# Kernel tuning notes

Measured on AMD Instinct MI355X. Metric: run time of the kernel, lower is better.

Reference implementation:

```python
import jax, jax.numpy as jnp
import numpy as np

B, H, W = 4, 256, 256
TARGET_BETA0 = 5
TARGET_LIFETIME = 0.5
LOSS_SCALE = 100.0


def setup_inputs() -> dict:
    key = jax.random.key(0)
    k1, k2 = jax.random.split(key)
    prob_map = jax.random.uniform(k1, (B, 1, H, W), dtype=jnp.float32)
    roi_mask = (jax.random.uniform(k2, (B, 1, H, W)) < 0.9).astype(jnp.float32)
    return {"prob_map": prob_map, "roi_mask": roi_mask}


def _ph0_topk_loss(f):
    """0-dim persistent homology (V-filtration, 4-connectivity) of f:[H,W],
    then standard top-k MSE(target_lifetime) loss. Equivalent to
    cripser.compute_ph_torch(f, maxdim=0, filtration='V') + _standard_loss.
    Algorithm: Kruskal over grid edges with weight max(f[u],f[v]), elder rule.
    All combinatorics run on stop_gradient values; births/deaths are
    differentiable gathers from f at the paired pixel indices."""
    Hh, Ww = f.shape
    N = Hh * Ww
    fv = f.reshape(-1)
    fvc = jax.lax.stop_gradient(fv)

    idx2d = jnp.arange(N, dtype=jnp.int32).reshape(Hh, Ww)
    r_u = idx2d[:, :-1].reshape(-1)  # right edges
    r_v = r_u + 1
    d_u = idx2d[:-1, :].reshape(-1)  # down edges
    d_v = d_u + Ww
    eu = jnp.concatenate([r_u, d_u])
    ev = jnp.concatenate([r_v, d_v])
    ew = jnp.maximum(fvc[eu], fvc[ev])
    order = jnp.argsort(ew)  # process edges by increasing filtration value
    eu, ev = eu[order], ev[order]

    parent0 = jnp.arange(N, dtype=jnp.int32)

    def step(parent, uv):
        u, v = uv[0], uv[1]

        def find(x):
            return jax.lax.while_loop(lambda y: parent[y] != y, lambda y: parent[y], x)

        ru = find(u)
        rv = find(v)
        merge = ru != rv
        # Invariant: a root is the argmin pixel of its component, so
        # fvc[root] is the component's birth value. Elder rule: the root
        # with smaller birth value survives (ties -> smaller index).
        older_u = (fvc[ru] < fvc[rv]) | ((fvc[ru] == fvc[rv]) & (ru < rv))
        keep = jnp.where(older_u, ru, rv)
        die = jnp.where(older_u, rv, ru)
        b_idx = jnp.where(merge, die, -1)  # birth pixel of the dying comp
        d_pix = jnp.where(fvc[u] >= fvc[v], u, v)  # death = max endpoint
        d_idx = jnp.where(merge, d_pix, -1)
        parent = parent.at[die].set(jnp.where(merge, keep, die))
        parent = parent.at[u].set(jnp.where(merge, keep, ru))  # path compression
        parent = parent.at[v].set(jnp.where(merge, keep, rv))
        return parent, (b_idx, d_idx)

    _, (pb, pd_) = jax.lax.scan(step, parent0, jnp.stack([eu, ev], axis=1))

    valid = pb >= 0
    births = fv[jnp.maximum(pb, 0)]
    deaths = fv[jnp.maximum(pd_, 0)]
    life = jnp.where(valid, deaths - births, 0.0)  # lifetimes >= 0

    # sort descending; invalid slots to the end (keys are stop-gradient)
    key_ = jnp.where(valid, jax.lax.stop_gradient(life), -jnp.inf)
    top = jnp.argsort(-key_)[:TARGET_BETA0]
    topk = life[top]
    vk = valid[top]
    n_use = jnp.sum(vk)  # = min(num_finite, target_beta0)
    sq = jnp.where(vk, (topk - TARGET_LIFETIME) ** 2, 0.0)
    return jnp.sum(sq) / jnp.maximum(n_use, 1).astype(f.dtype)


def reference(prob_map, roi_mask):
    prob = prob_map[:, 0] * roi_mask[:, 0]  # roi masking; (1-roi)*0 is a no-op
    filtration = 1.0 - prob
    losses = jax.vmap(_ph0_topk_loss)(filtration)
    return jnp.mean(losses) * LOSS_SCALE
```

## Files before the change

### kernel.cpp

```cpp
#include <hip/hip_runtime.h>
#include <stdint.h>

#define NPIX 65536
#define NRE  65280
#define NE   130560
#define NIMG 4
#define LTPB 1024
#define ETPB 1024
#define NBLK_L (NIMG*32)
#define TPIX 2048
#define EPAD 4096
#define KMAX 4096
#define HSZ  1024
#define LHSZ 2048
typedef unsigned long long u64;

__device__ __forceinline__ int ufind(unsigned* lbl, int x){
  int r = x, c = (int)lbl[r];
  while (c != r){ r = c; c = (int)lbl[r]; }
  while ((int)lbl[x] != r){ int n = (int)lbl[x]; lbl[x] = (unsigned)r; x = n; }
  return r;
}
__device__ __forceinline__ int ufind16(unsigned short* uf, int x){
  int r = x, c = (int)uf[r];
  while (c != r){ r = c; c = (int)uf[r]; }
  while ((int)uf[x] != r){ int n = (int)uf[x]; uf[x] = (unsigned short)r; x = n; }
  return r;
}

__device__ __forceinline__ void merge5(float* a, const float* b){
  float out[5]; int ia = 0, ib = 0;
  #pragma unroll
  for (int k = 0; k < 5; ++k){
    float av = (ia < 5) ? a[ia] : -2.0f;
    float bv = (ib < 5) ? b[ib] : -2.0f;
    if (av >= bv){ out[k] = av; ++ia; } else { out[k] = bv; ++ib; }
  }
  #pragma unroll
  for (int k = 0; k < 5; ++k) a[k] = out[k];
}

__global__ __launch_bounds__(LTPB)
void ph0_local(const float* __restrict__ prob, const float* __restrict__ roi,
               float* __restrict__ Fg, float* __restrict__ LIFEg,
               unsigned* __restrict__ LBLg, u64* __restrict__ LAg,
               unsigned* __restrict__ C, unsigned* __restrict__ C2,
               unsigned* __restrict__ MAPg, unsigned* __restrict__ KGg)
{
  const int blk = blockIdx.x;
  const int img = blk >> 5;
  const int tile = blk & 31;
  const int tr = tile >> 2, tc = tile & 3;
  const int gr0 = tr*32, gc0 = tc*64;
  const int tid = threadIdx.x;
  const int lane = tid & 63;

  const float* pm = prob + img*NPIX;
  const float* rm = roi  + img*NPIX;
  float* F = Fg + img*NPIX;
  float* LIFE = LIFEg + img*NPIX;
  unsigned* LBL = LBLg + img*NPIX;
  unsigned* MAP = MAPg + img*NPIX;
  unsigned* KG  = KGg  + img*NPIX;
  u64* LA = LAg + (size_t)img*NE;

  __shared__ float          sf[TPIX];
  __shared__ unsigned       slbl[TPIX];
  __shared__ unsigned       sme[TPIX];
  __shared__ unsigned short el[2][EPAD];
  __shared__ unsigned       aux[EPAD];
  __shared__ unsigned       bkw[192];
  __shared__ unsigned short bkp[192];
  __shared__ int s_n[3];

  for (int p = tid; p < TPIX; p += LTPB){
    int gp = ((gr0 + (p>>6))<<8) + gc0 + (p&63);
    float fv = 1.0f - pm[gp]*rm[gp];
    sf[p] = fv; slbl[p] = (unsigned)p;
    F[gp] = fv; LIFE[gp] = 0.0f;
  }
  if (tid < 3) s_n[tid] = 0;
  for (int s = tid; s < 192; s += LTPB){
    unsigned wv = 0xFFFFFFFFu; int p = 0; int gq = -1;
    if (s < 32){ if (tc > 0){ p = s*64;        gq = ((gr0+s)<<8)    + gc0 - 1;  } }
    else if (s < 64){ int k=s-32;  if (tc < 3){ p = k*64+63;  gq = ((gr0+k)<<8)  + gc0 + 64; } }
    else if (s < 128){ int k=s-64; if (tr > 0){ p = k;        gq = ((gr0-1)<<8)  + gc0 + k;  } }
    else { int k=s-128;            if (tr < 7){ p = 31*64+k;  gq = ((gr0+32)<<8) + gc0 + k;  } }
    if (gq >= 0){
      int gp = ((gr0 + (p>>6))<<8) + gc0 + (p&63);
      float fp = 1.0f - pm[gp]*rm[gp];
      float fq = 1.0f - pm[gq]*rm[gq];
      wv = __float_as_uint(fmaxf(fp, fq));
    }
    bkw[s] = wv; bkp[s] = (unsigned short)p;
  }
  __syncthreads();

  int M = EPAD, cur = 0;
  for (int rd = 0; rd < 100000; ++rd){
    int nxt = cur ^ 1;
    for (int i = tid; i < TPIX; i += LTPB) sme[i] = 0xFFFFFFFFu;
    if (tid == 0) s_n[(rd+1)%3] = 0;
    __syncthreads();
    if (tid < 192){
      unsigned wv = bkw[tid];
      if (wv != 0xFFFFFFFFu) atomicMin(&sme[ufind(slbl, (int)bkp[tid])], wv);
    }
    int Mpad = (M + 63) & ~63;
    for (int idx = tid; idx < Mpad; idx += LTPB){
      bool keep = false; int e=0,u=0,v=0,a=0,b=0;
      if (idx < M){
        e = (rd == 0) ? idx : (int)el[cur][idx];
        bool valid;
        if (e < 2048){ u=e; v=e+1; valid = ((e&63)!=63); }
        else { u=e-2048; v=u+64; valid = ((u>>6)!=31); }
        if (valid){
          a = ufind(slbl,u); b = ufind(slbl,v);
          if (a != b){
            unsigned wb = __float_as_uint(fmaxf(sf[u],sf[v]));
            atomicMin(&sme[a],wb); atomicMin(&sme[b],wb);
            keep = true;
          }
        }
      }
      u64 m = __ballot(keep);
      if (m){
        int pos0 = __popcll(m & ((1ULL<<lane)-1));
        int leader = __ffsll((long long)m)-1;
        int base = 0;
        if (lane == leader) base = atomicAdd(&s_n[rd%3], __popcll(m));
        base = __shfl(base, leader);
        if (keep){
          el[nxt][base+pos0] = (unsigned short)e;
          aux[base+pos0] = (unsigned)a | ((unsigned)b<<16);
        }
      }
    }
    __syncthreads();
    int n = s_n[rd%3];
    cur = nxt;
    if (n == M || n == 0){ M = n; break; }
    M = n;
    for (int idx = tid; idx < M; idx += LTPB){
      int e = (int)el[cur][idx];
      unsigned ab = aux[idx];
      int a = (int)(ab & 0xFFFFu), b = (int)(ab >> 16);
      int u, v;
      if (e < 2048){ u = e; v = e + 1; } else { u = e - 2048; v = u + 64; }
      float w = fmaxf(sf[u], sf[v]);
      unsigned wb = __float_as_uint(w);
      float fa = sf[a], fb = sf[b];
      bool bd = (fb < fa) || ((fb == fa) && (b < a));
      int die = bd ? a : b, keep = bd ? b : a;
      if (sme[die] == wb){
        slbl[die] = (unsigned)keep;
        int gd = ((gr0 + (die>>6))<<8) + gc0 + (die&63);
        LIFE[gd] = w - (bd ? fa : fb);
      }
    }
    __syncthreads();
  }

  for (int p = tid; p < TPIX; p += LTPB){
    int r = ufind(slbl, p);
    int gp = ((gr0 + (p>>6))<<8) + gc0 + (p&63);
    LBL[gp] = (unsigned)(((gr0 + (r>>6))<<8) + gc0 + (r&63));
  }
  __syncthreads();
  for (int p = tid; p < TPIX; p += LTPB){
    if ((int)slbl[p] == p){
      unsigned pos = atomicAdd(&C2[img], 1u);
      sme[p] = pos;
      unsigned gp = (unsigned)(((gr0 + (p>>6))<<8) + gc0 + (p&63));
      MAP[gp] = pos;
      KG[pos] = gp;
    }
  }
  __syncthreads();

  unsigned* hk = (unsigned*)&el[cur ^ 1][0];
  unsigned* hw = slbl;
  for (int i = tid; i < LHSZ; i += LTPB){ hk[i] = 0xFFFFFFFFu; hw[i] = 0xFFFFFFFFu; }
  __syncthreads();

  unsigned* ctr = &C[img];
  int Mpad2 = (M + 63) & ~63;
  for (int idx = tid; idx < Mpad2; idx += LTPB){
    bool spill = false;
    u64 rec = 0;
    if (idx < M){
      int e = (int)el[cur][idx];
      unsigned ab = aux[idx];
      int a = (int)(ab & 0xFFFFu), b = (int)(ab >> 16);
      int u, v;
      if (e < 2048){ u = e; v = e + 1; } else { u = e - 2048; v = u + 64; }
      unsigned wb = __float_as_uint(fmaxf(sf[u], sf[v]));
      int lo = a < b ? a : b, hi = a < b ? b : a;
      unsigned key = ((unsigned)lo << 11) | (unsigned)hi;
      unsigned h = ((key * 2654435761u) >> 21) & (LHSZ-1);
      bool ins = false;
      #pragma unroll
      for (int t = 0; t < 8; ++t){
        unsigned old = atomicCAS(&hk[h], 0xFFFFFFFFu, key);
        if (old == 0xFFFFFFFFu || old == key){ atomicMin(&hw[h], wb); ins = true; break; }
        h = (h + 1) & (LHSZ-1);
      }
      if (!ins){
        spill = true;
        rec = ((u64)wb << 32) | ((u64)sme[a] << 16) | sme[b];
      }
    }
    u64 m = __ballot(spill);
    if (m){
      int pos0 = __popcll(m & ((1ULL<<lane)-1));
      int leader = __ffsll((long long)m)-1;
      unsigned base = 0;
      if (lane == leader) base = atomicAdd(ctr, (unsigned)__popcll(m));
      base = (unsigned)__shfl((int)base, leader);
      if (spill) LA[base + pos0] = rec;
    }
  }
  __syncthreads();
  for (int h = tid; h < LHSZ; h += LTPB){
    unsigned key = hk[h];
    bool ok = (key != 0xFFFFFFFFu);
    u64 rec = 0;
    if (ok){
      int a = (int)(key >> 11), b = (int)(key & 0x7FFu);
      rec = ((u64)hw[h] << 32) | ((u64)sme[a] << 16) | sme[b];
    }
    u64 m = __ballot(ok);
    if (m){
      int pos0 = __popcll(m & ((1ULL<<lane)-1));
      int leader = __ffsll((long long)m)-1;
      unsigned base = 0;
      if (lane == leader) base = atomicAdd(ctr, (unsigned)__popcll(m));
      base = (unsigned)__shfl((int)base, leader);
      if (ok) LA[base + pos0] = rec;
    }
  }
}

#define RUN_ROUNDS_GLOBAL(UF, ME, RNK)                                       \
  for (int k = tid; k < K; k += ETPB){                                       \
    unsigned g = kg[k];                                                      \
    UF[k] = (unsigned short)k;                                               \
    RNK[k] = ((u64)__float_as_uint(f[g]) << 32) | g;                         \
  }                                                                          \
  __syncthreads();                                                           \
  for (int rd = 0; rd < 70000 && n > 0; ++rd){                               \
    for (int k = tid; k < K; k += ETPB) ME[k] = 0xFFFFFFFFu;                 \
    if (tid == 0) s_n[0] = 0;                                                \
    __syncthreads();                                                         \
    int Mpad = (n + 63) & ~63;                                               \
    for (int idx = tid; idx < Mpad; idx += ETPB){                            \
      bool keep = false; unsigned wb = 0; int a = 0, b = 0;                  \
      if (idx < n){                                                          \
        u64 rec = src[idx];                                                  \
        wb = (unsigned)(rec >> 32);                                          \
        a = (int)((rec >> 16) & 0xFFFFu);                                    \
        b = (int)(rec & 0xFFFFu);                                            \
        a = ufind16(UF, a); b = ufind16(UF, b);                              \
        if (a != b){ atomicMin(&ME[a], wb); atomicMin(&ME[b], wb); keep = true; } \
      }                                                                      \
      u64 m = __ballot(keep);                                                \
      if (m){                                                                \
        int pos0 = __popcll(m & ((1ULL<<lane)-1));                           \
        int leader = __ffsll((long long)m)-1;                                \
        int base = 0;                                                        \
        if (lane == leader) base = atomicAdd(&s_n[0], __popcll(m));          \
        base = __shfl(base, leader);                                         \
        if (keep) dst[base+pos0] = ((u64)wb<<32)|((u64)(unsigned)a<<16)|(unsigned)b; \
      }                                                                      \
    }                                                                        \
    __syncthreads();                                                         \
    int nn = s_n[0];                                                         \
    for (int idx = tid; idx < nn; idx += ETPB){                              \
      u64 rec = dst[idx];                                                    \
      unsigned wb = (unsigned)(rec >> 32);                                   \
      int a = (int)((rec >> 16) & 0xFFFFu);                                  \
      int b = (int)(rec & 0xFFFFu);                                          \
      bool bd = RNK[b] < RNK[a];                                             \
      int die = bd ? a : b, kp = bd ? b : a;                                 \
      if (ME[die] == wb){                                                    \
        UF[die] = (unsigned short)kp;                                        \
        u64 rk = RNK[die];                                                   \
        life[(unsigned)(rk & 0xFFFFFFFFu)] =                                 \
            __uint_as_float(wb) - __uint_as_float((unsigned)(rk >> 32));     \
      }                                                                      \
    }                                                                        \
    __syncthreads();                                                         \
    u64* t = src; src = dst; dst = t; n = nn;                                \
  }

__global__ __launch_bounds__(ETPB)
void ph0_endgame(const float* __restrict__ Fg, float* __restrict__ LIFEg,
                 unsigned* __restrict__ LBLg, unsigned* __restrict__ MAPg,
                 unsigned* __restrict__ KGg, u64* __restrict__ LAg,
                 u64* __restrict__ LBg, u64* __restrict__ GRg,
                 const unsigned* __restrict__ C, const unsigned* __restrict__ C2,
                 float* __restrict__ LOSS, unsigned* __restrict__ DONE,
                 float* __restrict__ out)
{
  const int img = blockIdx.x, tid = threadIdx.x;
  const int lane = tid & 63;
  const int wave = tid >> 6;
  const float* f = Fg + img*NPIX;
  float* life = LIFEg + img*NPIX;
  unsigned* lblg = LBLg + img*NPIX;
  unsigned* map  = MAPg + img*NPIX;
  const unsigned* kg = KGg + img*NPIX;
  u64* src = LAg + (size_t)img*NE;
  u64* dst = LBg + (size_t)img*NE;
  u64* rnk = GRg + (size_t)img*NPIX;

  __shared__ u64 smem8[7208];
  unsigned short* s_uf = (unsigned short*)smem8;
  unsigned* s_meB = (unsigned*)((char*)smem8 + 8192);
  unsigned* s_hkB = (unsigned*)((char*)smem8 + 40960);
  unsigned* s_hwB = (unsigned*)((char*)smem8 + 49152);
  float*    s_w5  = (float*)((char*)smem8 + 57344);
  __shared__ int s_n[3];

  const int K = (int)C2[img];
  const int nInt = (int)C[img];

  for (int s = tid; s < 2560; s += ETPB){
    int gu, gv;
    if (s < 768){ int ci = s >> 8, row = s & 255, col = 63 + (ci<<6); gu = (row<<8)+col; gv = gu+1; }
    else { int k = s - 768; int ri = k >> 8, colh = k & 255, gr = 31 + (ri<<5); gu = (gr<<8)+colh; gv = gu+256; }
    unsigned ia = map[lblg[gu]];
    unsigned ib = map[lblg[gv]];
    unsigned wb = __float_as_uint(fmaxf(f[gu], f[gv]));
    src[nInt + s] = ((u64)wb << 32) | ((u64)ia << 16) | ib;
  }
  if (tid < 3) s_n[tid] = 0;
  int n = nInt + 2560;

  if (K <= KMAX){
    for (int k = tid; k < K; k += ETPB){
      unsigned g = kg[k];
      s_uf[k] = (unsigned short)k;
      rnk[k] = ((u64)__float_as_uint(f[g]) << 32) | g;
      s_meB[k] = 0xFFFFFFFFu;
    }
    for (int h = tid; h < HSZ; h += ETPB){ s_hkB[h] = 0xFFFFFFFFu; s_hwB[h] = 0xFFFFFFFFu; }
    __syncthreads();

    for (int rd = 0; rd < 70000; ++rd){
      const int bi = rd & 1;
      unsigned* me = s_meB + bi*KMAX;
      unsigned* hk = s_hkB + bi*HSZ;
      unsigned* hw = s_hwB + bi*HSZ;
      const bool useHash = (n > 1024);
      int Mpad = (n + 63) & ~63;
      for (int idx = tid; idx < Mpad; idx += ETPB){
        bool app = false; unsigned wb = 0; int a = 0, b = 0;
        if (idx < n){
          u64 rec = src[idx];
          a = (int)((rec >> 16) & 0xFFFFu);
          b = (int)(rec & 0xFFFFu);
          a = ufind16(s_uf, a); b = ufind16(s_uf, b);
          if (a != b){
            wb = (unsigned)(rec >> 32);
            if (useHash){
              int lo = a < b ? a : b, hi = a < b ? b : a;
              unsigned key = ((unsigned)lo << 12) | (unsigned)hi;
              unsigned h = ((key * 2654435761u) >> 20) & (HSZ-1);
              bool ins = false;
              #pragma unroll
              for (int t = 0; t < 8; ++t){
                unsigned old = atomicCAS(&hk[h], 0xFFFFFFFFu, key);
                if (old == 0xFFFFFFFFu || old == key){ atomicMin(&hw[h], wb); ins = true; break; }
                h = (h + 1) & (HSZ-1);
              }
              if (!ins){ atomicMin(&me[a], wb); atomicMin(&me[b], wb); app = true; }
            } else {
              atomicMin(&me[a], wb); atomicMin(&me[b], wb); app = true;
            }
          }
        }
        u64 m = __ballot(app);
        if (m){
          int pos0 = __popcll(m & ((1ULL<<lane)-1));
          int leader = __ffsll((long long)m)-1;
          int base = 0;
          if (lane == leader) base = atomicAdd(&s_n[rd%3], __popcll(m));
          base = __shfl(base, leader);
          if (app) dst[base+pos0] = ((u64)wb<<32)|((u64)(unsigned)a<<16)|(unsigned)b;
        }
      }
      __syncthreads();
      if (useHash){
        for (int h = tid; h < HSZ; h += ETPB){
          unsigned key = hk[h];
          bool okk = (key != 0xFFFFFFFFu);
          unsigned wb = 0; int a = 0, b = 0;
          if (okk){
            a = (int)(key >> 12); b = (int)(key & 0xFFFu);
            wb = hw[h];
            atomicMin(&me[a], wb); atomicMin(&me[b], wb);
          }
          u64 m = __ballot(okk);
          if (m){
            int pos0 = __popcll(m & ((1ULL<<lane)-1));
            int leader = __ffsll((long long)m)-1;
            int base = 0;
            if (lane == leader) base = atomicAdd(&s_n[rd%3], __popcll(m));
            base = __shfl(base, leader);
            if (okk) dst[base+pos0] = ((u64)wb<<32)|((u64)(unsigned)a<<16)|(unsigned)b;
          }
        }
        __syncthreads();
      }
      int nn = s_n[rd%3];
      if (nn == 0) break;

      if (nn <= 64){
        unsigned* rwS = s_meB + (bi^1)*KMAX;
        for (int k = tid; k < K; k += ETPB) rwS[k] = (unsigned)(rnk[k] >> 32);
        __syncthreads();
        if (wave == 0){
          u64 rec = (lane < nn) ? dst[lane] : 0;
          bool alive = (lane < nn);
          unsigned wb = (unsigned)(rec >> 32);
          int a = (int)((rec >> 16) & 0xFFFFu);
          int b = (int)(rec & 0xFFFFu);
          for (int g = 0; g < 100000; ++g){
            if (alive){
              a = ufind16(s_uf, a); b = ufind16(s_uf, b);
              if (a == b) alive = false;
            }
            if (__ballot(alive) == 0ULL) break;
            if (alive){ me[a] = 0xFFFFFFFFu; me[b] = 0xFFFFFFFFu; }
            __threadfence_block();
            if (alive){ atomicMin(&me[a], wb); atomicMin(&me[b], wb); }
            __threadfence_block();
            if (alive){
              unsigned ra = rwS[a], rb = rwS[b];
              bool bd = (rb < ra) || ((rb == ra) && (b < a));
              int die = bd ? a : b, kp = bd ? b : a;
              if (me[die] == wb){
                s_uf[die] = (unsigned short)kp;
                life[kg[die]] = __uint_as_float(wb) - __uint_as_float(rwS[die]);
              }
            }
            __threadfence_block();
          }
        }
        break;
      }

      for (int idx = tid; idx < nn; idx += ETPB){
        u64 rec = dst[idx];
        unsigned wb = (unsigned)(rec >> 32);
        int a = (int)((rec >> 16) & 0xFFFFu);
        int b = (int)(rec & 0xFFFFu);
        u64 ra = rnk[a], rb = rnk[b];
        bool bd = rb < ra;
        int die = bd ? a : b, kp = bd ? b : a;
        if (me[die] == wb){
          s_uf[die] = (unsigned short)kp;
          u64 rk = bd ? ra : rb;
          life[(unsigned)(rk & 0xFFFFFFFFu)] =
              __uint_as_float(wb) - __uint_as_float((unsigned)(rk >> 32));
        }
      }
      {
        unsigned* meN = s_meB + (bi^1)*KMAX;
        for (int k = tid; k < K; k += ETPB) meN[k] = 0xFFFFFFFFu;
        if (nn > 1024){
          unsigned* hkN = s_hkB + (bi^1)*HSZ;
          unsigned* hwN = s_hwB + (bi^1)*HSZ;
          for (int h = tid; h < HSZ; h += ETPB){ hkN[h] = 0xFFFFFFFFu; hwN[h] = 0xFFFFFFFFu; }
        }
        if (tid == 0) s_n[(rd+1)%3] = 0;
      }
      __syncthreads();
      u64* t = src; src = dst; dst = t;
      n = nn;
    }
  } else {
    __syncthreads();
    unsigned short* g_uf = (unsigned short*)lblg;
    unsigned*       g_me = map;
    u64*            g_rnk = rnk;
    RUN_ROUNDS_GLOBAL(g_uf, g_me, g_rnk)
  }
  __syncthreads();

  float t5[5] = {-1.f,-1.f,-1.f,-1.f,-1.f};
  for (int i = tid; i < NPIX; i += ETPB){
    float v = life[i];
    if (v > t5[4]){
      int j = 4;
      while (j > 0 && t5[j-1] < v){ t5[j] = t5[j-1]; --j; }
      t5[j] = v;
    }
  }
  #pragma unroll
  for (int off = 1; off < 64; off <<= 1){
    float o[5];
    #pragma unroll
    for (int k = 0; k < 5; ++k) o[k] = __shfl_xor(t5[k], off);
    merge5(t5, o);
  }
  if (lane == 0){
    int wv = tid >> 6;
    #pragma unroll
    for (int k = 0; k < 5; ++k) s_w5[wv*5+k] = t5[k];
  }
  __syncthreads();
  if (tid < 64){
    float u5[5];
    #pragma unroll
    for (int k = 0; k < 5; ++k) u5[k] = (tid < ETPB/64) ? s_w5[tid*5+k] : -2.0f;
    #pragma unroll
    for (int off = 1; off < 16; off <<= 1){
      float o[5];
      #pragma unroll
      for (int k = 0; k < 5; ++k) o[k] = __shfl_xor(u5[k], off);
      merge5(u5, o);
    }
    if (tid == 0){
      float lsum = 0.0f;
      #pragma unroll
      for (int k = 0; k < 5; ++k){ float d = u5[k] - 0.5f; lsum += d*d; }
      atomicExch(&LOSS[img], lsum * 0.2f);
      __threadfence();
      unsigned prev = atomicAdd(DONE, 1u);
      if (prev == NIMG - 1){
        float s = 0.0f;
        #pragma unroll
        for (int i = 0; i < NIMG; ++i) s += atomicAdd(&LOSS[i], 0.0f);
        out[0] = s * 25.0f;
      }
    }
  }
}

extern "C" void kernel_launch(void* const* d_in, const int* in_sizes, int n_in,
                              void* d_out, int out_size, void* d_ws, size_t ws_size,
                              hipStream_t stream)
{
  const float* prob = (const float*)d_in[0];
  const float* roi  = (const float*)d_in[1];
  char* ws = (char*)d_ws;
  const size_t SZL = (size_t)4*NE*8;
  float*    F    = (float*)(ws);
  float*    LIFE = (float*)(ws + (1u<<20));
  unsigned* LBL  = (unsigned*)(ws + (2u<<20));
  unsigned* MAP  = (unsigned*)(ws + (3u<<20));
  unsigned* KG   = (unsigned*)(ws + (4u<<20));
  u64*      LA   = (u64*)(ws + (5u<<20));
  u64*      LB   = (u64*)(ws + (5u<<20) + SZL);
  u64*      GR   = (u64*)(ws + (5u<<20) + 2*SZL);
  unsigned* C    = (unsigned*)(ws + (5u<<20) + 2*SZL + (2u<<20));
  unsigned* C2   = C + 4;
  unsigned* DONE = C + 8;
  float*    LOSS = (float*)((char*)C + 64);
  float*    out  = (float*)d_out;

  hipMemsetAsync(C, 0, 64, stream);
  ph0_local<<<NBLK_L, LTPB, 0, stream>>>(prob, roi, F, LIFE, LBL, LA, C, C2, MAP, KG);
  ph0_endgame<<<NIMG, ETPB, 0, stream>>>(F, LIFE, LBL, MAP, KG, LA, LB, GR, C, C2, LOSS, DONE, out);
}
```

Baseline: 316.3 us.

## Finish small residual edge sets with sorted single-wave Kruskal instead of Boruvka rounds

```diff
diff --git a/kernel.cpp b/kernel.cpp
--- a/kernel.cpp
+++ b/kernel.cpp
@@ -13,6 +13,7 @@
 #define KMAX 4096
 #define HSZ  1024
 #define LHSZ 2048
+#define SCAP 2048
 typedef unsigned long long u64;
 
 __device__ __forceinline__ int ufind(unsigned* lbl, int x){
@@ -320,6 +321,9 @@
   unsigned* s_hkB = (unsigned*)((char*)smem8 + 40960);
   unsigned* s_hwB = (unsigned*)((char*)smem8 + 49152);
   float*    s_w5  = (float*)((char*)smem8 + 57344);
+  unsigned* s_claim = s_meB;
+  u64*      s_srt   = (u64*)((char*)smem8 + 8192 + 16384);
+  unsigned* s_bw    = (unsigned*)((char*)smem8 + 40960);
   __shared__ int s_n[3];
 
   const int K = (int)C2[img];
@@ -347,12 +351,12 @@
     for (int h = tid; h < HSZ; h += ETPB){ s_hkB[h] = 0xFFFFFFFFu; s_hwB[h] = 0xFFFFFFFFu; }
     __syncthreads();
 
+    int m = 0;
     for (int rd = 0; rd < 70000; ++rd){
       const int bi = rd & 1;
       unsigned* me = s_meB + bi*KMAX;
       unsigned* hk = s_hkB + bi*HSZ;
       unsigned* hw = s_hwB + bi*HSZ;
-      const bool useHash = (n > 1024);
       int Mpad = (n + 63) & ~63;
       for (int idx = tid; idx < Mpad; idx += ETPB){
         bool app = false; unsigned wb = 0; int a = 0, b = 0;
@@ -363,94 +367,52 @@
           a = ufind16(s_uf, a); b = ufind16(s_uf, b);
           if (a != b){
             wb = (unsigned)(rec >> 32);
-            if (useHash){
-              int lo = a < b ? a : b, hi = a < b ? b : a;
-              unsigned key = ((unsigned)lo << 12) | (unsigned)hi;
-              unsigned h = ((key * 2654435761u) >> 20) & (HSZ-1);
-              bool ins = false;
-              #pragma unroll
-              for (int t = 0; t < 8; ++t){
-                unsigned old = atomicCAS(&hk[h], 0xFFFFFFFFu, key);
-                if (old == 0xFFFFFFFFu || old == key){ atomicMin(&hw[h], wb); ins = true; break; }
-                h = (h + 1) & (HSZ-1);
-              }
-              if (!ins){ atomicMin(&me[a], wb); atomicMin(&me[b], wb); app = true; }
-            } else {
-              atomicMin(&me[a], wb); atomicMin(&me[b], wb); app = true;
+            int lo = a < b ? a : b, hi = a < b ? b : a;
+            unsigned key = ((unsigned)lo << 12) | (unsigned)hi;
+            unsigned h = ((key * 2654435761u) >> 20) & (HSZ-1);
+            bool ins = false;
+            #pragma unroll
+            for (int t = 0; t < 8; ++t){
+              unsigned old = atomicCAS(&hk[h], 0xFFFFFFFFu, key);
+              if (old == 0xFFFFFFFFu || old == key){ atomicMin(&hw[h], wb); ins = true; break; }
+              h = (h + 1) & (HSZ-1);
             }
+            if (!ins){ atomicMin(&me[a], wb); atomicMin(&me[b], wb); app = true; }
           }
         }
-        u64 m = __ballot(app);
-        if (m){
-          int pos0 = __popcll(m & ((1ULL<<lane)-1));
-          int leader = __ffsll((long long)m)-1;
+        u64 mm = __ballot(app);
+        if (mm){
+          int pos0 = __popcll(mm & ((1ULL<<lane)-1));
+          int leader = __ffsll((long long)mm)-1;
           int base = 0;
-          if (lane == leader) base = atomicAdd(&s_n[rd%3], __popcll(m));
+          if (lane == leader) base = atomicAdd(&s_n[rd%3], __popcll(mm));
           base = __shfl(base, leader);
           if (app) dst[base+pos0] = ((u64)wb<<32)|((u64)(unsigned)a<<16)|(unsigned)b;
         }
       }
       __syncthreads();
-      if (useHash){
-        for (int h = tid; h < HSZ; h += ETPB){
-          unsigned key = hk[h];
-          bool okk = (key != 0xFFFFFFFFu);
-          unsigned wb = 0; int a = 0, b = 0;
-          if (okk){
-            a = (int)(key >> 12); b = (int)(key & 0xFFFu);
-            wb = hw[h];
-            atomicMin(&me[a], wb); atomicMin(&me[b], wb);
-          }
-          u64 m = __ballot(okk);
-          if (m){
-            int pos0 = __popcll(m & ((1ULL<<lane)-1));
-            int leader = __ffsll((long long)m)-1;
-            int base = 0;
-            if (lane == leader) base = atomicAdd(&s_n[rd%3], __popcll(m));
-            base = __shfl(base, leader);
-            if (okk) dst[base+pos0] = ((u64)wb<<32)|((u64)(unsigned)a<<16)|(unsigned)b;
-          }
-        }
-        __syncthreads();
-      }
+      for (int h = tid; h < HSZ; h += ETPB){
+        unsigned key = hk[h];
+        bool okk = (key != 0xFFFFFFFFu);
+        unsigned wb = 0; int a = 0, b = 0;
+        if (okk){
+          a = (int)(key >> 12); b = (int)(key & 0xFFFu);
+          wb = hw[h];
+          atomicMin(&me[a], wb); atomicMin(&me[b], wb);
+        }
+        u64 mm = __ballot(okk);
+        if (mm){
+          int pos0 = __popcll(mm & ((1ULL<<lane)-1));
+          int leader = __ffsll((long long)mm)-1;
+          int base = 0;
+          if (lane == leader) base = atomicAdd(&s_n[rd%3], __popcll(mm));
+          base = __shfl(base, leader);
+          if (okk) dst[base+pos0] = ((u64)wb<<32)|((u64)(unsigned)a<<16)|(unsigned)b;
+        }
+      }
+      __syncthreads();
       int nn = s_n[rd%3];
-      if (nn == 0) break;
-
-      if (nn <= 64){
-        unsigned* rwS = s_meB + (bi^1)*KMAX;
-        for (int k = tid; k < K; k += ETPB) rwS[k] = (unsigned)(rnk[k] >> 32);
-        __syncthreads();
-        if (wave == 0){
-          u64 rec = (lane < nn) ? dst[lane] : 0;
-          bool alive = (lane < nn);
-          unsigned wb = (unsigned)(rec >> 32);
-          int a = (int)((rec >> 16) & 0xFFFFu);
-          int b = (int)(rec & 0xFFFFu);
-          for (int g = 0; g < 100000; ++g){
-            if (alive){
-              a = ufind16(s_uf, a); b = ufind16(s_uf, b);
-              if (a == b) alive = false;
-            }
-            if (__ballot(alive) == 0ULL) break;
-            if (alive){ me[a] = 0xFFFFFFFFu; me[b] = 0xFFFFFFFFu; }
-            __threadfence_block();
-            if (alive){ atomicMin(&me[a], wb); atomicMin(&me[b], wb); }
-            __threadfence_block();
-            if (alive){
-              unsigned ra = rwS[a], rb = rwS[b];
-              bool bd = (rb < ra) || ((rb == ra) && (b < a));
-              int die = bd ? a : b, kp = bd ? b : a;
-              if (me[die] == wb){
-                s_uf[die] = (unsigned short)kp;
-                life[kg[die]] = __uint_as_float(wb) - __uint_as_float(rwS[die]);
-              }
-            }
-            __threadfence_block();
-          }
-        }
-        break;
-      }
-
+      if (nn <= SCAP){ m = nn; break; }
       for (int idx = tid; idx < nn; idx += ETPB){
         u64 rec = dst[idx];
         unsigned wb = (unsigned)(rec >> 32);
@@ -469,23 +431,82 @@
       {
         unsigned* meN = s_meB + (bi^1)*KMAX;
         for (int k = tid; k < K; k += ETPB) meN[k] = 0xFFFFFFFFu;
-        if (nn > 1024){
-          unsigned* hkN = s_hkB + (bi^1)*HSZ;
-          unsigned* hwN = s_hwB + (bi^1)*HSZ;
-          for (int h = tid; h < HSZ; h += ETPB){ hkN[h] = 0xFFFFFFFFu; hwN[h] = 0xFFFFFFFFu; }
-        }
+        unsigned* hkN = s_hkB + (bi^1)*HSZ;
+        unsigned* hwN = s_hwB + (bi^1)*HSZ;
+        for (int h = tid; h < HSZ; h += ETPB){ hkN[h] = 0xFFFFFFFFu; hwN[h] = 0xFFFFFFFFu; }
         if (tid == 0) s_n[(rd+1)%3] = 0;
       }
       __syncthreads();
       u64* t = src; src = dst; dst = t;
       n = nn;
     }
+
+    __syncthreads();
+    for (int k = tid; k < KMAX; k += ETPB){
+      s_claim[k] = 0xFFFFFFFFu;
+      if (k < K) s_bw[k] = (unsigned)(rnk[k] >> 32);
+    }
+    for (int i = tid; i < SCAP; i += ETPB) s_srt[i] = (i < m) ? dst[i] : ~0ULL;
+    __syncthreads();
+    if (wave == 0 && m > 0){
+      for (unsigned k2 = 2; k2 <= SCAP; k2 <<= 1){
+        for (unsigned j = k2 >> 1; j > 0; j >>= 1){
+          for (int t = lane; t < SCAP; t += 64){
+            int ixj = t ^ (int)j;
+            if (ixj > t){
+              u64 x = s_srt[t], y = s_srt[ixj];
+              bool up = ((t & k2) == 0);
+              if ((x > y) == up){ s_srt[t] = y; s_srt[ixj] = x; }
+            }
+          }
+          __threadfence_block();
+        }
+      }
+      unsigned epoch = 0;
+      for (int base = 0; base < m; base += 64){
+        int i = base + lane;
+        bool alive = (i < m);
+        unsigned wb = 0; int a = 0, b = 0;
+        if (alive){
+          u64 rec = s_srt[i];
+          wb = (unsigned)(rec >> 32);
+          a = (int)((rec >> 16) & 0xFFFFu);
+          b = (int)(rec & 0xFFFFu);
+        }
+        for (int si = 0; si < 100; ++si){
+          if (alive){
+            a = ufind16(s_uf, a); b = ufind16(s_uf, b);
+            if (a == b) alive = false;
+          }
+          if (__ballot(alive) == 0ULL) break;
+          ++epoch;
+          unsigned mykey = ((0x00FFFFFFu - epoch) << 8) | (unsigned)lane;
+          if (alive){ atomicMin(&s_claim[a], mykey); atomicMin(&s_claim[b], mykey); }
+          __threadfence_block();
+          if (alive && s_claim[a] == mykey && s_claim[b] == mykey){
+            unsigned ba = s_bw[a], bb = s_bw[b];
+            bool bd = (bb < ba) || ((bb == ba) && (b < a));
+            int die = bd ? a : b, kp = bd ? b : a;
+            s_uf[die] = (unsigned short)kp;
+            u64 rk = rnk[die];
+            life[(unsigned)(rk & 0xFFFFFFFFu)] =
+                __uint_as_float(wb) - __uint_as_float((unsigned)(rk >> 32));
+            alive = false;
+          }
+          __threadfence_block();
+        }
+      }
+    }
+    __syncthreads();
+    if (tid == 0) life[kg[ufind16(s_uf, 0)]] = 0.0f;
   } else {
     __syncthreads();
     unsigned short* g_uf = (unsigned short*)lblg;
     unsigned*       g_me = map;
     u64*            g_rnk = rnk;
     RUN_ROUNDS_GLOBAL(g_uf, g_me, g_rnk)
+    __syncthreads();
+    if (tid == 0) life[kg[ufind16(g_uf, 0)]] = 0.0f;
   }
   __syncthreads();
 
```

Result: slower. 610.9 us (+93.1%).
